# Optimization experiments

Hardware: AMD Instinct MI355X
Metric: run time of the kernel (lower is better)

The kernel has to match this reference:

```python
import jax, jax.numpy as jnp
import numpy as np

N_NODES = 100000
N_EDGES = 3200000
ALPHA = 0.1
ITERATIONS = 10


def setup_inputs() -> dict:
    key = jax.random.key(0)
    ks = jax.random.split(key, 7)
    features = jax.random.normal(ks[0], (N_NODES, 512), dtype=jnp.float32)
    W1 = jax.random.normal(ks[1], (512, 64), dtype=jnp.float32) * 0.05
    b1 = jax.random.normal(ks[2], (64,), dtype=jnp.float32) * 0.05
    W2 = jax.random.normal(ks[3], (64, 64), dtype=jnp.float32) * 0.05
    b2 = jax.random.normal(ks[4], (64,), dtype=jnp.float32) * 0.05
    edge_weights = jax.random.uniform(ks[5], (N_EDGES,), dtype=jnp.float32)
    edge_index = jax.random.randint(ks[6], (2, N_EDGES), 0, N_NODES, dtype=jnp.int64)
    return {"features": features, "W1": W1, "b1": b1, "W2": W2, "b2": b2,
            "edge_weights": edge_weights, "edge_index": edge_index}


def reference(features, W1, b1, W2, b2, edge_weights, edge_index):
    # dense MLP head (dropout disabled / eval mode)
    h = jax.nn.relu(features @ W1 + b1)          # [N, hidden]
    z = h @ W2 + b2                              # [N, labels]

    row, col = edge_index[0], edge_index[1]

    def step(p, _):
        # SpMM: out[row] += w * p[col]
        gathered = edge_weights[:, None] * p[col]                 # [E, labels]
        new = jax.ops.segment_sum(gathered, row, num_segments=N_NODES)
        p = (1.0 - ALPHA) * new + ALPHA * z
        return p, None

    p, _ = jax.lax.scan(step, z, None, length=ITERATIONS)
    return p
```

## Files before the change

kernel.cpp:

```cpp
#include <hip/hip_runtime.h>
#include <hip/hip_fp16.h>
#include <cmath>

#define N_NODES 100000
#define N_EDGES 3200000
#define ALPHA   0.1f
#define ITERS   10
#define NBUK    1024
#define RPB     98
#define CHUNK   16384
#define NCH     196

typedef __attribute__((ext_vector_type(8))) short short8;
typedef __attribute__((ext_vector_type(4))) float f32x4;

__device__ __forceinline__ short f2bf(float x) {
    union { float f; unsigned u; } v; v.f = x;
    unsigned r = v.u + 0x7fffu + ((v.u >> 16) & 1u);
    return (short)(r >> 16);
}

__global__ void prep_w(const float* __restrict__ W1, const float* __restrict__ W2,
                       short* __restrict__ W1t, short* __restrict__ W2t)
{
    int t = blockIdx.x * 256 + threadIdx.x;
    if (t < 512 * 64) { int k = t >> 6, c = t & 63; W1t[c * 512 + k] = f2bf(W1[t]); }
    if (t < 64 * 64)  { int k = t >> 6, c = t & 63; W2t[c * 64 + k]  = f2bf(W2[t]); }
}

__global__ __launch_bounds__(256) void mlp_mfma(
    const float* __restrict__ F, const short* __restrict__ W1t,
    const short* __restrict__ W2t, const float* __restrict__ b1,
    const float* __restrict__ b2, __half* __restrict__ q0)
{
    __shared__ short Ft[64 * 128];
    __shared__ short Ht[64 * 64];

    const int t  = threadIdx.x;
    const int l  = t & 63;
    const int wv = t >> 6;
    const int wr = wv * 16;
    const long base = (long)blockIdx.x * 64;

    const int sr = t >> 4;
    const int sk = (t & 15) * 8;

    float4 f0a, f0b, f1a, f1b, f2a, f2b, f3a, f3b;

#define LOAD_TILE(kt) do {                                                   \
    long g0 = base + sr;      if (g0 > N_NODES - 1) g0 = N_NODES - 1;        \
    long g1 = base + sr + 16; if (g1 > N_NODES - 1) g1 = N_NODES - 1;        \
    long g2 = base + sr + 32; if (g2 > N_NODES - 1) g2 = N_NODES - 1;        \
    long g3 = base + sr + 48; if (g3 > N_NODES - 1) g3 = N_NODES - 1;        \
    f0a = *(const float4*)(F + g0 * 512 + (kt) * 128 + sk);                  \
    f0b = *(const float4*)(F + g0 * 512 + (kt) * 128 + sk + 4);              \
    f1a = *(const float4*)(F + g1 * 512 + (kt) * 128 + sk);                  \
    f1b = *(const float4*)(F + g1 * 512 + (kt) * 128 + sk + 4);              \
    f2a = *(const float4*)(F + g2 * 512 + (kt) * 128 + sk);                  \
    f2b = *(const float4*)(F + g2 * 512 + (kt) * 128 + sk + 4);              \
    f3a = *(const float4*)(F + g3 * 512 + (kt) * 128 + sk);                  \
    f3b = *(const float4*)(F + g3 * 512 + (kt) * 128 + sk + 4);              \
} while (0)

#define STORE_ROW(row, fa, fb) do {                                          \
    int r_ = (row);                                                          \
    short8 s_ = { f2bf((fa).x), f2bf((fa).y), f2bf((fa).z), f2bf((fa).w),    \
                  f2bf((fb).x), f2bf((fb).y), f2bf((fb).z), f2bf((fb).w) };  \
    *(short8*)&Ft[(r_ * 128 + sk) ^ ((r_ & 7) << 3)] = s_;                   \
} while (0)

    LOAD_TILE(0);

    f32x4 acc[4] = {};
    for (int kt = 0; kt < 4; ++kt) {
        STORE_ROW(sr,      f0a, f0b);
        STORE_ROW(sr + 16, f1a, f1b);
        STORE_ROW(sr + 32, f2a, f2b);
        STORE_ROW(sr + 48, f3a, f3b);
        __syncthreads();
        if (kt < 3) LOAD_TILE(kt + 1);
#pragma unroll
        for (int kc = 0; kc < 4; ++kc) {
            int kb = kc * 32 + (l >> 4) * 8;
            int ar = wr + (l & 15);
            short8 a = *(const short8*)&Ft[(ar * 128 + kb) ^ ((ar & 7) << 3)];
#pragma unroll
            for (int n = 0; n < 4; ++n) {
                int bc = n * 16 + (l & 15);
                short8 b = *(const short8*)(W1t + bc * 512 + kt * 128 + kb);
                acc[n] = __builtin_amdgcn_mfma_f32_16x16x32_bf16(a, b, acc[n], 0, 0, 0);
            }
        }
        __syncthreads();
    }

#pragma unroll
    for (int n = 0; n < 4; ++n) {
        int col = n * 16 + (l & 15);
        float bv = b1[col];
#pragma unroll
        for (int i = 0; i < 4; ++i) {
            int row = wr + (l >> 4) * 4 + i;
            float hv = fmaxf(acc[n][i] + bv, 0.0f);
            Ht[(row * 64 + col) ^ ((row & 7) << 3)] = f2bf(hv);
        }
    }
    f32x4 acc2[4] = {};
#pragma unroll
    for (int kc = 0; kc < 2; ++kc) {
        int kb = kc * 32 + (l >> 4) * 8;
        int ar = wr + (l & 15);
        short8 a = *(const short8*)&Ht[(ar * 64 + kb) ^ ((ar & 7) << 3)];
#pragma unroll
        for (int n = 0; n < 4; ++n) {
            int bc = n * 16 + (l & 15);
            short8 b = *(const short8*)(W2t + bc * 64 + kb);
            acc2[n] = __builtin_amdgcn_mfma_f32_16x16x32_bf16(a, b, acc2[n], 0, 0, 0);
        }
    }
#pragma unroll
    for (int n = 0; n < 4; ++n) {
        int col = n * 16 + (l & 15);
        float bv = b2[col];
#pragma unroll
        for (int i = 0; i < 4; ++i) {
            long row = base + wr + (l >> 4) * 4 + i;
            if (row < N_NODES)
                q0[row * 64 + col] = __float2half(acc2[n][i] + bv);
        }
    }
#undef LOAD_TILE
#undef STORE_ROW
}

__global__ __launch_bounds__(256) void bhist(const int* __restrict__ rows, int* __restrict__ gh)
{
    __shared__ int cnt[NBUK];
    for (int i = threadIdx.x; i < NBUK; i += 256) cnt[i] = 0;
    __syncthreads();
    int base = blockIdx.x * CHUNK;
    int end  = base + CHUNK; if (end > N_EDGES) end = N_EDGES;
    for (int i = base + threadIdx.x; i < end; i += 256)
        atomicAdd(&cnt[rows[i] / RPB], 1);
    __syncthreads();
    for (int i = threadIdx.x; i < NBUK; i += 256)
        gh[i * NCH + blockIdx.x] = cnt[i];
}

__global__ __launch_bounds__(512) void bscan(int* __restrict__ gh, int* __restrict__ btot)
{
    __shared__ int s[512];
    int k = blockIdx.x;
    int t = threadIdx.x;
    int v = (t < NCH) ? gh[k * NCH + t] : 0;
    s[t] = v;
    __syncthreads();
    for (int off = 1; off < 512; off <<= 1) {
        int x = (t >= off) ? s[t - off] : 0;
        __syncthreads();
        s[t] += x;
        __syncthreads();
    }
    if (t < NCH) gh[k * NCH + t] = s[t] - v;
    if (t == NCH - 1) btot[k] = s[t];
}

__global__ __launch_bounds__(1024) void scan_btot(const int* __restrict__ btot, int* __restrict__ bbase)
{
    __shared__ int s[1024];
    int t = threadIdx.x;
    int v = btot[t];
    s[t] = v;
    __syncthreads();
    for (int off = 1; off < 1024; off <<= 1) {
        int x = (t >= off) ? s[t - off] : 0;
        __syncthreads();
        s[t] += x;
        __syncthreads();
    }
    bbase[t] = s[t] - v;
}

__global__ __launch_bounds__(256) void bpart(const int* __restrict__ rows, const int* __restrict__ cols,
                                             const float* __restrict__ w, const int* __restrict__ gh,
                                             const int* __restrict__ bbase, uint2* __restrict__ stg)
{
    __shared__ int cur[NBUK];
    int blk = blockIdx.x;
    for (int i = threadIdx.x; i < NBUK; i += 256)
        cur[i] = bbase[i] + gh[i * NCH + blk];
    __syncthreads();
    int base = blk * CHUNK;
    int end  = base + CHUNK; if (end > N_EDGES) end = N_EDGES;
    for (int i = base + threadIdx.x; i < end; i += 256) {
        int r = rows[i];
        int b = r / RPB;
        int pos = atomicAdd(&cur[b], 1);
        float ws = w[i] * ((1.0f - ALPHA) / 16.0f);
        unsigned meta = (unsigned)cols[i] | ((unsigned)(r - b * RPB) << 17);
        stg[pos] = make_uint2(meta, __float_as_uint(ws));
    }
}

__global__ __launch_bounds__(256) void bucket_sort2(const int* __restrict__ bbase,
                                                    const uint2* __restrict__ stg,
                                                    unsigned long long* __restrict__ cw,
                                                    int* __restrict__ rowp)
{
    __shared__ int ldeg[RPB];
    __shared__ int lcur[RPB];
    __shared__ int sc[128];
    const int b = blockIdx.x;
    const int rowlo = b * RPB;
    if (rowlo >= N_NODES) return;
    int rowhi = rowlo + RPB; if (rowhi > N_NODES) rowhi = N_NODES;
    const int nrows = rowhi - rowlo;
    const int t = threadIdx.x;
    const int base = bbase[b];
    const int cnt = ((b + 1 < NBUK) ? bbase[b + 1] : N_EDGES) - base;

    if (t < RPB) ldeg[t] = 0;
    __syncthreads();
    for (int j = t; j < cnt; j += 256)
        atomicAdd(&ldeg[stg[base + j].x >> 17], 1);
    __syncthreads();
    int v = 0;
    if (t < 128) { v = (t < nrows) ? ldeg[t] : 0; sc[t] = v; }
    __syncthreads();
    for (int off = 1; off < 128; off <<= 1) {
        int x = (t < 128 && t >= off) ? sc[t - off] : 0;
        __syncthreads();
        if (t < 128) sc[t] += x;
        __syncthreads();
    }
    if (t < nrows) {
        int rp = base + sc[t] - v;
        rowp[rowlo + t] = rp;
        lcur[t] = rp;
    }
    if (t == 0 && rowhi == N_NODES) rowp[N_NODES] = base + cnt;
    __syncthreads();
    for (int j = t; j < cnt; j += 256) {
        uint2 rec = stg[base + j];
        int roff = rec.x >> 17;
        unsigned col = rec.x & 0x1FFFFu;
        int pos = atomicAdd(&lcur[roff], 1);
        cw[pos] = (unsigned long long)col | ((unsigned long long)rec.y << 32);
    }
}

template <int LAST>
__global__ __launch_bounds__(256) void spmm_kernel(
    const int* __restrict__ rowp, const unsigned long long* __restrict__ cw,
    const __half* __restrict__ qin, const __half* __restrict__ zh,
    float beta, float outscale,
    __half* __restrict__ qout, float* __restrict__ out)
{
    const int wid = blockIdx.x * 4 + (threadIdx.x >> 6);
    if (wid >= N_NODES) return;
    const int lane = threadIdx.x & 63;
    const int sub  = lane >> 3;
    const int l8   = lane & 7;

    const int start = rowp[wid];
    const int end   = rowp[wid + 1];

    uint4 zv = *(const uint4*)(zh + (long)wid * 64 + l8 * 8);

    float a0 = 0, a1 = 0, a2 = 0, a3 = 0, a4 = 0, a5 = 0, a6 = 0, a7 = 0;

#define ACC_EDGE(pc, v)                                                       \
    do {                                                                      \
        float ww_ = __uint_as_float((unsigned)((pc) >> 32));                  \
        float2 p_;                                                            \
        p_ = __half22float2(*(__half2*)&(v).x); a0 += ww_ * p_.x; a1 += ww_ * p_.y; \
        p_ = __half22float2(*(__half2*)&(v).y); a2 += ww_ * p_.x; a3 += ww_ * p_.y; \
        p_ = __half22float2(*(__half2*)&(v).z); a4 += ww_ * p_.x; a5 += ww_ * p_.y; \
        p_ = __half22float2(*(__half2*)&(v).w); a6 += ww_ * p_.x; a7 += ww_ * p_.y; \
    } while (0)

    int e = start + sub;
    for (; e + 24 < end; e += 32) {
        unsigned long long pc0 = cw[e];
        unsigned long long pc1 = cw[e + 8];
        unsigned long long pc2 = cw[e + 16];
        unsigned long long pc3 = cw[e + 24];
        uint4 v0 = *(const uint4*)(qin + (long)(unsigned)pc0 * 64 + l8 * 8);
        uint4 v1 = *(const uint4*)(qin + (long)(unsigned)pc1 * 64 + l8 * 8);
        uint4 v2 = *(const uint4*)(qin + (long)(unsigned)pc2 * 64 + l8 * 8);
        uint4 v3 = *(const uint4*)(qin + (long)(unsigned)pc3 * 64 + l8 * 8);
        ACC_EDGE(pc0, v0);
        ACC_EDGE(pc1, v1);
        ACC_EDGE(pc2, v2);
        ACC_EDGE(pc3, v3);
    }
    for (; e < end; e += 8) {
        unsigned long long pc = cw[e];
        uint4 v = *(const uint4*)(qin + (long)(unsigned)pc * 64 + l8 * 8);
        ACC_EDGE(pc, v);
    }
#undef ACC_EDGE

    a0 += __shfl_xor(a0, 8);  a1 += __shfl_xor(a1, 8);
    a2 += __shfl_xor(a2, 8);  a3 += __shfl_xor(a3, 8);
    a4 += __shfl_xor(a4, 8);  a5 += __shfl_xor(a5, 8);
    a6 += __shfl_xor(a6, 8);  a7 += __shfl_xor(a7, 8);
    a0 += __shfl_xor(a0, 16); a1 += __shfl_xor(a1, 16);
    a2 += __shfl_xor(a2, 16); a3 += __shfl_xor(a3, 16);
    a4 += __shfl_xor(a4, 16); a5 += __shfl_xor(a5, 16);
    a6 += __shfl_xor(a6, 16); a7 += __shfl_xor(a7, 16);
    a0 += __shfl_xor(a0, 32); a1 += __shfl_xor(a1, 32);
    a2 += __shfl_xor(a2, 32); a3 += __shfl_xor(a3, 32);
    a4 += __shfl_xor(a4, 32); a5 += __shfl_xor(a5, 32);
    a6 += __shfl_xor(a6, 32); a7 += __shfl_xor(a7, 32);

    if (lane < 8) {
        float2 z0 = __half22float2(*(__half2*)&zv.x);
        float2 z1 = __half22float2(*(__half2*)&zv.y);
        float2 z2 = __half22float2(*(__half2*)&zv.z);
        float2 z3 = __half22float2(*(__half2*)&zv.w);
        float o0 = a0 + beta * z0.x, o1 = a1 + beta * z0.y;
        float o2 = a2 + beta * z1.x, o3 = a3 + beta * z1.y;
        float o4 = a4 + beta * z2.x, o5 = a5 + beta * z2.y;
        float o6 = a6 + beta * z3.x, o7 = a7 + beta * z3.y;
        if (LAST) {
            float4 ra = { outscale * o0, outscale * o1, outscale * o2, outscale * o3 };
            float4 rb = { outscale * o4, outscale * o5, outscale * o6, outscale * o7 };
            *(float4*)(out + (long)wid * 64 + lane * 8)     = ra;
            *(float4*)(out + (long)wid * 64 + lane * 8 + 4) = rb;
        } else {
            __half2 h0 = __floats2half2_rn(o0, o1);
            __half2 h1 = __floats2half2_rn(o2, o3);
            __half2 h2 = __floats2half2_rn(o4, o5);
            __half2 h3 = __floats2half2_rn(o6, o7);
            uint4 pv = { *(unsigned*)&h0, *(unsigned*)&h1, *(unsigned*)&h2, *(unsigned*)&h3 };
            *(uint4*)(qout + (long)wid * 64 + lane * 8) = pv;
        }
    }
}

extern "C" void kernel_launch(void* const* d_in, const int* in_sizes, int n_in,
                              void* d_out, int out_size, void* d_ws, size_t ws_size,
                              hipStream_t stream)
{
    const float* features = (const float*)d_in[0];
    const float* W1 = (const float*)d_in[1];
    const float* b1 = (const float*)d_in[2];
    const float* W2 = (const float*)d_in[3];
    const float* b2 = (const float*)d_in[4];
    const float* ew = (const float*)d_in[5];
    const int*   ei = (const int*)d_in[6];
    const int* erow = ei;
    const int* ecol = ei + N_EDGES;
    float* out = (float*)d_out;

    char* ws = (char*)d_ws;
    size_t off = 0;
    auto alloc = [&](size_t bytes) {
        size_t c = off;
        off += (bytes + 255) & ~(size_t)255;
        return c;
    };
    __half* q0    = (__half*)(ws + alloc((size_t)N_NODES * 64 * 2));
    __half* qA    = (__half*)(ws + alloc((size_t)N_NODES * 64 * 2));
    __half* qB    = (__half*)(ws + alloc((size_t)N_NODES * 64 * 2));
    unsigned long long* cw = (unsigned long long*)(ws + alloc((size_t)N_EDGES * 8));
    uint2* stg    = (uint2*)(ws + alloc((size_t)N_EDGES * 8));
    int*   gh     = (int*)  (ws + alloc((size_t)NBUK * NCH * 4));
    short* W1t    = (short*)(ws + alloc((size_t)512 * 64 * 2));
    short* W2t    = (short*)(ws + alloc((size_t)64 * 64 * 2));
    int*   rowp   = (int*)  (ws + alloc((size_t)(N_NODES + 1) * 4));
    int*   btot   = (int*)  (ws + alloc((size_t)NBUK * 4));
    int*   bbase  = (int*)  (ws + alloc((size_t)NBUK * 4));
    (void)ws_size; (void)in_sizes; (void)n_in; (void)out_size;

    prep_w<<<128, 256, 0, stream>>>(W1, W2, W1t, W2t);
    mlp_mfma<<<(N_NODES + 63) / 64, 256, 0, stream>>>(features, W1t, W2t, b1, b2, q0);

    bhist<<<NCH, 256, 0, stream>>>(erow, gh);
    bscan<<<NBUK, 512, 0, stream>>>(gh, btot);
    scan_btot<<<1, 1024, 0, stream>>>(btot, bbase);
    bpart<<<NCH, 256, 0, stream>>>(erow, ecol, ew, gh, bbase, stg);
    bucket_sort2<<<NBUK, 256, 0, stream>>>(bbase, stg, cw, rowp);

    const __half* qi = q0;
    for (int it = 1; it < ITERS; ++it) {
        __half* qo = (it & 1) ? qA : qB;
        float beta = (float)(0.1 / pow(16.0, (double)it));
        spmm_kernel<0><<<(N_NODES + 3) / 4, 256, 0, stream>>>(rowp, cw, qi, q0, beta, 1.0f, qo, nullptr);
        qi = qo;
    }
    float beta10 = (float)(0.1 / pow(16.0, 10.0));
    float osc    = (float)pow(16.0, 10.0);
    spmm_kernel<1><<<(N_NODES + 3) / 4, 256, 0, stream>>>(rowp, cw, qi, q0, beta10, osc, nullptr, out);
}
```

Measured before the change: 802.8 us.

## Split SpMM rows across 16 lanes per edge with 8-byte gathers; halve chunk size

The SpMM kernel now assigns 16 lanes per edge, each loading 4 half values (8 bytes), so a wave handles 4 edges at once instead of 8 lanes × 8 halves handling 8 edges. This lowers register use per lane and shortens the shuffle reduction, but each gather instruction moves half as many bytes. The unroll depth per iteration also drops from 4 to 2 edges per sub-group, which reduces memory-level parallelism. Separately, the preprocessing chunk size is halved and the chunk count doubled.

```diff
diff --git a/kernel.cpp b/kernel.cpp
--- a/kernel.cpp
+++ b/kernel.cpp
@@ -8,8 +8,8 @@
 #define ITERS   10
 #define NBUK    1024
 #define RPB     98
-#define CHUNK   16384
-#define NCH     196
+#define CHUNK   8192
+#define NCH     391
 
 typedef __attribute__((ext_vector_type(8))) short short8;
 typedef __attribute__((ext_vector_type(4))) float f32x4;
@@ -259,15 +259,15 @@
     const int wid = blockIdx.x * 4 + (threadIdx.x >> 6);
     if (wid >= N_NODES) return;
     const int lane = threadIdx.x & 63;
-    const int sub  = lane >> 3;
-    const int l8   = lane & 7;
+    const int sub  = lane >> 4;
+    const int l16  = lane & 15;
 
     const int start = rowp[wid];
     const int end   = rowp[wid + 1];
 
-    uint4 zv = *(const uint4*)(zh + (long)wid * 64 + l8 * 8);
-
-    float a0 = 0, a1 = 0, a2 = 0, a3 = 0, a4 = 0, a5 = 0, a6 = 0, a7 = 0;
+    uint2 zv = *(const uint2*)(zh + (long)wid * 64 + l16 * 4);
+
+    float a0 = 0, a1 = 0, a2 = 0, a3 = 0;
 
 #define ACC_EDGE(pc, v)                                                       \
     do {                                                                      \
@@ -275,66 +275,42 @@
         float2 p_;                                                            \
         p_ = __half22float2(*(__half2*)&(v).x); a0 += ww_ * p_.x; a1 += ww_ * p_.y; \
         p_ = __half22float2(*(__half2*)&(v).y); a2 += ww_ * p_.x; a3 += ww_ * p_.y; \
-        p_ = __half22float2(*(__half2*)&(v).z); a4 += ww_ * p_.x; a5 += ww_ * p_.y; \
-        p_ = __half22float2(*(__half2*)&(v).w); a6 += ww_ * p_.x; a7 += ww_ * p_.y; \
     } while (0)
 
     int e = start + sub;
-    for (; e + 24 < end; e += 32) {
+    for (; e + 4 < end; e += 8) {
         unsigned long long pc0 = cw[e];
-        unsigned long long pc1 = cw[e + 8];
-        unsigned long long pc2 = cw[e + 16];
-        unsigned long long pc3 = cw[e + 24];
-        uint4 v0 = *(const uint4*)(qin + (long)(unsigned)pc0 * 64 + l8 * 8);
-        uint4 v1 = *(const uint4*)(qin + (long)(unsigned)pc1 * 64 + l8 * 8);
-        uint4 v2 = *(const uint4*)(qin + (long)(unsigned)pc2 * 64 + l8 * 8);
-        uint4 v3 = *(const uint4*)(qin + (long)(unsigned)pc3 * 64 + l8 * 8);
+        unsigned long long pc1 = cw[e + 4];
+        uint2 v0 = *(const uint2*)(qin + (long)(unsigned)pc0 * 64 + l16 * 4);
+        uint2 v1 = *(const uint2*)(qin + (long)(unsigned)pc1 * 64 + l16 * 4);
         ACC_EDGE(pc0, v0);
         ACC_EDGE(pc1, v1);
-        ACC_EDGE(pc2, v2);
-        ACC_EDGE(pc3, v3);
-    }
-    for (; e < end; e += 8) {
+    }
+    if (e < end) {
         unsigned long long pc = cw[e];
-        uint4 v = *(const uint4*)(qin + (long)(unsigned)pc * 64 + l8 * 8);
+        uint2 v = *(const uint2*)(qin + (long)(unsigned)pc * 64 + l16 * 4);
         ACC_EDGE(pc, v);
     }
 #undef ACC_EDGE
 
-    a0 += __shfl_xor(a0, 8);  a1 += __shfl_xor(a1, 8);
-    a2 += __shfl_xor(a2, 8);  a3 += __shfl_xor(a3, 8);
-    a4 += __shfl_xor(a4, 8);  a5 += __shfl_xor(a5, 8);
-    a6 += __shfl_xor(a6, 8);  a7 += __shfl_xor(a7, 8);
     a0 += __shfl_xor(a0, 16); a1 += __shfl_xor(a1, 16);
     a2 += __shfl_xor(a2, 16); a3 += __shfl_xor(a3, 16);
-    a4 += __shfl_xor(a4, 16); a5 += __shfl_xor(a5, 16);
-    a6 += __shfl_xor(a6, 16); a7 += __shfl_xor(a7, 16);
     a0 += __shfl_xor(a0, 32); a1 += __shfl_xor(a1, 32);
     a2 += __shfl_xor(a2, 32); a3 += __shfl_xor(a3, 32);
-    a4 += __shfl_xor(a4, 32); a5 += __shfl_xor(a5, 32);
-    a6 += __shfl_xor(a6, 32); a7 += __shfl_xor(a7, 32);
-
-    if (lane < 8) {
+
+    if (lane < 16) {
         float2 z0 = __half22float2(*(__half2*)&zv.x);
         float2 z1 = __half22float2(*(__half2*)&zv.y);
-        float2 z2 = __half22float2(*(__half2*)&zv.z);
-        float2 z3 = __half22float2(*(__half2*)&zv.w);
         float o0 = a0 + beta * z0.x, o1 = a1 + beta * z0.y;
         float o2 = a2 + beta * z1.x, o3 = a3 + beta * z1.y;
-        float o4 = a4 + beta * z2.x, o5 = a5 + beta * z2.y;
-        float o6 = a6 + beta * z3.x, o7 = a7 + beta * z3.y;
         if (LAST) {
-            float4 ra = { outscale * o0, outscale * o1, outscale * o2, outscale * o3 };
-            float4 rb = { outscale * o4, outscale * o5, outscale * o6, outscale * o7 };
-            *(float4*)(out + (long)wid * 64 + lane * 8)     = ra;
-            *(float4*)(out + (long)wid * 64 + lane * 8 + 4) = rb;
+            float4 r = { outscale * o0, outscale * o1, outscale * o2, outscale * o3 };
+            *(float4*)(out + (long)wid * 64 + l16 * 4) = r;
         } else {
             __half2 h0 = __floats2half2_rn(o0, o1);
             __half2 h1 = __floats2half2_rn(o2, o3);
-            __half2 h2 = __floats2half2_rn(o4, o5);
-            __half2 h3 = __floats2half2_rn(o6, o7);
-            uint4 pv = { *(unsigned*)&h0, *(unsigned*)&h1, *(unsigned*)&h2, *(unsigned*)&h3 };
-            *(uint4*)(qout + (long)wid * 64 + lane * 8) = pv;
+            uint2 pv = { *(unsigned*)&h0, *(unsigned*)&h1 };
+            *(uint2*)(qout + (long)wid * 64 + l16 * 4) = pv;
         }
     }
 }
```

After: 876.1 us. 9.1% more time.
